# Optimization experiments

Hardware: AMD Instinct MI355X
Metric: run time of the kernel (lower is better)

The kernel has to match this reference:

```python
import jax, jax.numpy as jnp
import numpy as np

TOP_K = 20
BN_EPS = 1e-5

B, F, D, O = 2048, 16384, 512, 4096


def setup_inputs() -> dict:
    key = jax.random.key(0)
    ks = jax.random.split(key, 4)
    return {
        "sae_features": jax.random.uniform(ks[0], (B, F), jnp.float32),  # nonneg SAE activations
        "emb": jax.random.normal(ks[1], (F, D), jnp.float32) * (1.0 / np.sqrt(D)),
        "lin_w": jax.random.normal(ks[2], (O, F), jnp.float32) * (1.0 / np.sqrt(F)),
        "lin_b": jnp.zeros((O,), jnp.float32),
        "global_bias": jnp.zeros((O,), jnp.float32),
        "bn1_gamma": jnp.ones((D,), jnp.float32),
        "bn1_beta": jnp.zeros((D,), jnp.float32),
        "mlp_w1": jax.random.normal(ks[3], (D, D), jnp.float32) * np.sqrt(2.0 / D),
        "mlp_b1": jnp.zeros((D,), jnp.float32),
        "bn2_gamma": jnp.ones((D,), jnp.float32),
        "bn2_beta": jnp.zeros((D,), jnp.float32),
        "mlp_w2": jax.random.normal(jax.random.fold_in(key, 7), (O, D), jnp.float32) * np.sqrt(2.0 / D),
        "mlp_b2": jnp.zeros((O,), jnp.float32),
    }


def _batchnorm(x, gamma, beta):
    # training-mode BatchNorm1d: biased batch statistics, eps=1e-5
    mean = jnp.mean(x, axis=0)
    var = jnp.var(x, axis=0)
    return (x - mean) * jax.lax.rsqrt(var + BN_EPS) * gamma + beta


def reference(sae_features, emb, lin_w, lin_b, global_bias, bn1_gamma, bn1_beta,
              mlp_w1, mlp_b1, bn2_gamma, bn2_beta, mlp_w2, mlp_b2):
    b = sae_features.shape[0]
    # --- top-k sparsification (keep top 20 activations per row, zero the rest) ---
    top_vals, top_idx = jax.lax.top_k(sae_features, TOP_K)  # [B, K]
    x = jnp.zeros_like(sae_features).at[jnp.arange(b)[:, None], top_idx].set(top_vals)
    # --- bi-interaction pooling: 0.5*((x@E)^2 - (x^2)@(E^2)) ---
    # algebraically identical to the broadcast multiply-sum in the source
    sum_emb = x @ emb                      # [B, D]
    sum_sq = (x * x) @ (emb * emb)          # [B, D]
    bi = 0.5 * (sum_emb * sum_emb - sum_sq)
    # --- BN + interaction MLP (dropout = identity in eval) ---
    h = _batchnorm(bi, bn1_gamma, bn1_beta)
    h = h @ mlp_w1.T + mlp_b1
    h = jax.nn.relu(_batchnorm(h, bn2_gamma, bn2_beta))
    interaction_out = h @ mlp_w2.T + mlp_b2  # [B, O]
    # --- linear component on the ORIGINAL (non-sparsified) features ---
    linear_out = sae_features @ lin_w.T + lin_b  # [B, O]
    output = global_bias[None, :] + linear_out + interaction_out
    return output, linear_out, interaction_out
```

## Files before the change

kernel.cpp:

```cpp
#include <hip/hip_runtime.h>

#define B_ 2048
#define F_ 16384
#define D_ 512
#define O_ 4096

typedef __attribute__((ext_vector_type(8))) short bf16x8;
typedef __attribute__((ext_vector_type(4))) float f32x4;
typedef unsigned long long ull;

__device__ inline unsigned short f2bf(float f) {
    unsigned u = __float_as_uint(f);
    u += 0x7FFFu + ((u >> 16) & 1u);
    return (unsigned short)(u >> 16);
}

__device__ inline void glds16(const void* g, void* l) {
    __builtin_amdgcn_global_load_lds((const __attribute__((address_space(1))) void*)g,
                                     (__attribute__((address_space(3))) void*)l, 16, 0, 0);
}

__device__ inline void cvt_span(const float* __restrict__ s, unsigned short* __restrict__ d,
                                int n4, int tid0, int stride) {
    for (int i = tid0; i < n4; i += stride) {
        float4 v = ((const float4*)s)[i];
        ushort4 o;
        o.x = f2bf(v.x); o.y = f2bf(v.y); o.z = f2bf(v.z); o.w = f2bf(v.w);
        ((ushort4*)d)[i] = o;
    }
}

#define TOPK_BLKS (8 * B_)
#define CVT_BLKS  4096
__global__ __launch_bounds__(256) void fused_front_kernel(
        const float* __restrict__ sae, ull* __restrict__ cand,
        unsigned short* __restrict__ sae_bf,
        const float* __restrict__ lin_w, unsigned short* __restrict__ linw_bf,
        const float* __restrict__ w1, unsigned short* __restrict__ w1_bf,
        const float* __restrict__ w2, unsigned short* __restrict__ w2_bf) {
    __shared__ ull maxk[256];
    __shared__ ull cbuf[160];
    int tid = threadIdx.x;
    int bidx = blockIdx.x;
    if (bidx >= TOPK_BLKS) {
        int cb = bidx - TOPK_BLKS;
        int tid0 = cb * 256 + tid;
        int stride = CVT_BLKS * 256;
        cvt_span(lin_w, linw_bf, (int)((size_t)O_ * F_ / 4), tid0, stride);
        cvt_span(w1, w1_bf, D_ * D_ / 4, tid0, stride);
        cvt_span(w2, w2_bf, O_ * D_ / 4, tid0, stride);
        return;
    }
    int chunk = bidx & 7, row = bidx >> 3;
    size_t rbase = (size_t)row * F_ + chunk * 2048;
    const float4* src4 = (const float4*)(sae + rbase);
    ushort4* dst4 = (ushort4*)(sae_bf + rbase);

    float4 va = src4[tid], vb = src4[tid + 256];
    ushort4 oa, ob;
    oa.x = f2bf(va.x); oa.y = f2bf(va.y); oa.z = f2bf(va.z); oa.w = f2bf(va.w);
    ob.x = f2bf(vb.x); ob.y = f2bf(vb.y); ob.z = f2bf(vb.z); ob.w = f2bf(vb.w);
    dst4[tid] = oa; dst4[tid + 256] = ob;

    int c0 = chunk * 2048 + 4 * tid;
#define MKKEY(v, c) ((((ull)__float_as_uint(v)) << 32) | (unsigned)(~(c)))
    ull k0 = MKKEY(va.x, c0 + 0), k1 = MKKEY(va.y, c0 + 1);
    ull k2 = MKKEY(va.z, c0 + 2), k3 = MKKEY(va.w, c0 + 3);
    ull k4 = MKKEY(vb.x, c0 + 1024), k5 = MKKEY(vb.y, c0 + 1025);
    ull k6 = MKKEY(vb.z, c0 + 1026), k7 = MKKEY(vb.w, c0 + 1027);
#undef MKKEY
#define CE(a, b) { ull x_ = a, y_ = b; ull h_ = x_ > y_ ? x_ : y_; ull l_ = x_ > y_ ? y_ : x_; a = h_; b = l_; }
    CE(k0,k1) CE(k2,k3) CE(k4,k5) CE(k6,k7)
    CE(k0,k2) CE(k1,k3) CE(k4,k6) CE(k5,k7)
    CE(k1,k2) CE(k5,k6)
    CE(k0,k4) CE(k1,k5) CE(k2,k6) CE(k3,k7)
    CE(k2,k4) CE(k3,k5)
    CE(k1,k2) CE(k3,k4) CE(k5,k6)
#undef CE

    maxk[tid] = k0;
    __syncthreads();
    int r = 0;
    for (int k = 0; k < 256; ++k) r += (maxk[k] > k0);
    if (r < 20) {
        ull* o = cbuf + r * 8;
        o[0]=k0; o[1]=k1; o[2]=k2; o[3]=k3; o[4]=k4; o[5]=k5; o[6]=k6; o[7]=k7;
    }
    __syncthreads();
    ull myc = (tid < 160) ? cbuf[tid] : 0ull;
    int r2 = 0;
    for (int k = 0; k < 160; ++k) r2 += (cbuf[k] > myc);
    if (tid < 160 && r2 < 20)
        cand[((size_t)row * 8 + chunk) * 20 + r2] = myc;
}

__global__ __launch_bounds__(256) void bi_kernel(const ull* __restrict__ cand,
        const float* __restrict__ emb, float* __restrict__ bi) {
    __shared__ ull c[160];
    __shared__ int   si[20];
    __shared__ float sv[20];
    int tid = threadIdx.x, row = blockIdx.x;
    if (tid < 160) c[tid] = cand[(size_t)row * 160 + tid];
    __syncthreads();
    if (tid < 160) {
        ull m = c[tid];
        int r = 0;
        for (int k = 0; k < 160; ++k) r += (c[k] > m);
        if (r < 20) {
            sv[r] = __uint_as_float((unsigned)(m >> 32));
            si[r] = (int)(~(unsigned)m);
        }
    }
    __syncthreads();
    float s0 = 0.f, q0 = 0.f, s1 = 0.f, q1 = 0.f;
    int d0 = tid, d1 = tid + 256;
#pragma unroll
    for (int k = 0; k < 20; ++k) {
        float v = sv[k];
        const float* e = emb + (size_t)si[k] * D_;
        float e0 = e[d0], e1 = e[d1];
        s0 += v * e0; q0 += v * v * e0 * e0;
        s1 += v * e1; q1 += v * v * e1 * e1;
    }
    bi[(size_t)row * D_ + d0] = 0.5f * (s0 * s0 - q0);
    bi[(size_t)row * D_ + d1] = 0.5f * (s1 * s1 - q1);
}

__global__ __launch_bounds__(256) void colpart_kernel(const float* __restrict__ X,
        float* __restrict__ ps, float* __restrict__ pq, int N) {
    __shared__ float4 ls[128], lq[128];
    int tid = threadIdx.x;
    int c4 = tid & 127, half = tid >> 7;
    int r0 = blockIdx.x * 32 + half;
    float4 s = {0.f, 0.f, 0.f, 0.f}, q = {0.f, 0.f, 0.f, 0.f};
#pragma unroll
    for (int i = 0; i < 16; ++i) {
        float4 x = ((const float4*)(X + (size_t)(r0 + 2 * i) * N))[c4];
        s.x += x.x; s.y += x.y; s.z += x.z; s.w += x.w;
        q.x += x.x * x.x; q.y += x.y * x.y; q.z += x.z * x.z; q.w += x.w * x.w;
    }
    if (half) { ls[c4] = s; lq[c4] = q; }
    __syncthreads();
    if (!half) {
        float4 s2 = ls[c4], q2 = lq[c4];
        s.x += s2.x; s.y += s2.y; s.z += s2.z; s.w += s2.w;
        q.x += q2.x; q.y += q2.y; q.z += q2.z; q.w += q2.w;
        ((float4*)(ps + (size_t)blockIdx.x * N))[c4] = s;
        ((float4*)(pq + (size_t)blockIdx.x * N))[c4] = q;
    }
}

__global__ __launch_bounds__(256) void colfin_kernel(const float* __restrict__ ps,
        const float* __restrict__ pq, const float* __restrict__ gamma,
        const float* __restrict__ beta, float* __restrict__ scale,
        float* __restrict__ shift, int npart, int N, int M) {
    int col = blockIdx.x * 256 + threadIdx.x;
    if (col >= N) return;
    float s = 0.f, q = 0.f;
    for (int k = 0; k < npart; ++k) {
        s += ps[(size_t)k * N + col];
        q += pq[(size_t)k * N + col];
    }
    float mean = s / M;
    float var = q / M - mean * mean;
    float sc = gamma[col] * rsqrtf(var + 1e-5f);
    scale[col] = sc;
    shift[col] = beta[col] - mean * sc;
}

__global__ void bn_apply_kernel(const float* __restrict__ X, const float* __restrict__ scale,
        const float* __restrict__ shift, unsigned short* __restrict__ Y,
        int n4, int colmask4, int relu) {
    int stride = gridDim.x * blockDim.x;
    for (int i = blockIdx.x * blockDim.x + threadIdx.x; i < n4; i += stride) {
        float4 x = ((const float4*)X)[i];
        int c = (i & colmask4) * 4;
        float4 sc = *(const float4*)(scale + c);
        float4 sh = *(const float4*)(shift + c);
        float y0 = x.x * sc.x + sh.x;
        float y1 = x.y * sc.y + sh.y;
        float y2 = x.z * sc.z + sh.z;
        float y3 = x.w * sc.w + sh.w;
        if (relu) {
            y0 = fmaxf(y0, 0.f); y1 = fmaxf(y1, 0.f);
            y2 = fmaxf(y2, 0.f); y3 = fmaxf(y3, 0.f);
        }
        ushort4 o;
        o.x = f2bf(y0); o.y = f2bf(y1); o.z = f2bf(y2); o.w = f2bf(y3);
        ((ushort4*)Y)[i] = o;
    }
}

template <bool FUSE>
__global__ __launch_bounds__(512) void gemm8w_kernel(const unsigned short* __restrict__ A,
        const unsigned short* __restrict__ W, const float* __restrict__ bias,
        float* __restrict__ out, const float* __restrict__ lin,
        const float* __restrict__ gb, float* __restrict__ out0,
        int M, int N, int K) {
    __shared__ short As[3 * 4096];
    __shared__ short Bs[3 * 4096];
    int tid = threadIdx.x;
    int lane = tid & 63, w = tid >> 6;
    int wr = w >> 2, wc = w & 3;
    int l15 = lane & 15, lhi = lane >> 4;
    int xk = (l15 >> 1) & 3;
    int rchunk = (lhi ^ xk) << 3;

    int nwg = gridDim.x * gridDim.y;
    int bid = blockIdx.y * gridDim.x + blockIdx.x;
    int s = (bid & 7) * (nwg >> 3) + (bid >> 3);
    int gsz = gridDim.x << 3;
    int g = s / gsz, r = s % gsz;
    int by = (g << 3) + (r & 7);
    int bx = r >> 3;
    int bm = by * 128, bn = bx * 128;

    int rA = tid >> 2;
    int kp = tid & 3;
    int kps = kp ^ ((rA >> 1) & 3);
    const unsigned short* gA = A + (size_t)(bm + rA) * K + kps * 8;
    const unsigned short* gB = W + (size_t)(bn + rA) * K + kps * 8;

    f32x4 acc[4][2];
#pragma unroll
    for (int i = 0; i < 4; ++i)
#pragma unroll
        for (int j = 0; j < 2; ++j) { f32x4 z = {0.f, 0.f, 0.f, 0.f}; acc[i][j] = z; }

    auto STAGE = [&](int t, int buf) {
        int k0 = t << 5;
        glds16(gA + k0, (char*)(As + buf * 4096) + w * 1024);
        glds16(gB + k0, (char*)(Bs + buf * 4096) + w * 1024);
    };
    auto LOADF = [&](bf16x8* af, bf16x8* bv, int buf) {
        const short* Ab = As + buf * 4096;
        const short* Bb = Bs + buf * 4096;
#pragma unroll
        for (int mi = 0; mi < 4; ++mi)
            af[mi] = *(const bf16x8*)&Ab[(wr * 64 + mi * 16 + l15) * 32 + rchunk];
#pragma unroll
        for (int ni = 0; ni < 2; ++ni)
            bv[ni] = *(const bf16x8*)&Bb[(wc * 32 + ni * 16 + l15) * 32 + rchunk];
    };
    auto MFMA8 = [&](const bf16x8* af, const bf16x8* bv) {
#pragma unroll
        for (int mi = 0; mi < 4; ++mi)
#pragma unroll
            for (int ni = 0; ni < 2; ++ni)
                acc[mi][ni] = __builtin_amdgcn_mfma_f32_16x16x32_bf16(af[mi], bv[ni], acc[mi][ni], 0, 0, 0);
    };

    int NT = K >> 5;

    STAGE(0, 0);
    STAGE(1, 1);
    asm volatile("s_waitcnt vmcnt(2)" ::: "memory");
    __builtin_amdgcn_sched_barrier(0);
    __builtin_amdgcn_s_barrier();
    __builtin_amdgcn_sched_barrier(0);

    bf16x8 afA[4], bvA[2], afB[4], bvB[2];
    LOADF(afA, bvA, 0);

    for (int t = 0; t + 4 <= NT; t += 2) {
        STAGE(t + 2, (t + 2) % 3);
        asm volatile("s_waitcnt lgkmcnt(0)" ::: "memory");
        __builtin_amdgcn_sched_barrier(0);
        asm volatile("s_waitcnt vmcnt(2)" ::: "memory");
        __builtin_amdgcn_sched_barrier(0);
        __builtin_amdgcn_s_barrier();
        __builtin_amdgcn_sched_barrier(0);
        LOADF(afB, bvB, (t + 1) % 3);
        __builtin_amdgcn_s_setprio(1);
        MFMA8(afA, bvA);
        __builtin_amdgcn_s_setprio(0);
        __builtin_amdgcn_sched_group_barrier(0x100, 6, 0);
        __builtin_amdgcn_sched_group_barrier(0x008, 8, 0);
        STAGE(t + 3, (t + 3) % 3);
        asm volatile("s_waitcnt lgkmcnt(0)" ::: "memory");
        __builtin_amdgcn_sched_barrier(0);
        asm volatile("s_waitcnt vmcnt(2)" ::: "memory");
        __builtin_amdgcn_sched_barrier(0);
        __builtin_amdgcn_s_barrier();
        __builtin_amdgcn_sched_barrier(0);
        LOADF(afA, bvA, (t + 2) % 3);
        __builtin_amdgcn_s_setprio(1);
        MFMA8(afB, bvB);
        __builtin_amdgcn_s_setprio(0);
        __builtin_amdgcn_sched_group_barrier(0x100, 6, 0);
        __builtin_amdgcn_sched_group_barrier(0x008, 8, 0);
    }
    asm volatile("s_waitcnt lgkmcnt(0)" ::: "memory");
    __builtin_amdgcn_sched_barrier(0);
    asm volatile("s_waitcnt vmcnt(0)" ::: "memory");
    __builtin_amdgcn_sched_barrier(0);
    __builtin_amdgcn_s_barrier();
    __builtin_amdgcn_sched_barrier(0);
    LOADF(afB, bvB, (NT - 1) % 3);
    __builtin_amdgcn_s_setprio(1);
    MFMA8(afA, bvA);
    __builtin_amdgcn_s_setprio(0);
    asm volatile("s_waitcnt lgkmcnt(0)" ::: "memory");
    __builtin_amdgcn_sched_barrier(0);
    __builtin_amdgcn_s_setprio(1);
    MFMA8(afB, bvB);
    __builtin_amdgcn_s_setprio(0);

#pragma unroll
    for (int mi = 0; mi < 4; ++mi)
#pragma unroll
        for (int ni = 0; ni < 2; ++ni) {
            int col = bn + wc * 32 + ni * 16 + l15;
            float bb = bias[col];
            float gbv = FUSE ? gb[col] : 0.f;
            int row0 = bm + wr * 64 + mi * 16 + lhi * 4;
#pragma unroll
            for (int r2 = 0; r2 < 4; ++r2) {
                size_t idx = (size_t)(row0 + r2) * N + col;
                float v = acc[mi][ni][r2] + bb;
                out[idx] = v;
                if (FUSE) out0[idx] = gbv + lin[idx] + v;
            }
        }
}

template <bool FUSE>
__global__ __launch_bounds__(512) void gemm256_kernel(const unsigned short* __restrict__ A,
        const unsigned short* __restrict__ W, const float* __restrict__ bias,
        float* __restrict__ out, const float* __restrict__ lin,
        const float* __restrict__ gb, float* __restrict__ out0,
        int M, int N, int K) {
    __shared__ short As[3 * 16384];
    __shared__ short Bs[3 * 8192];
    int tid = threadIdx.x;
    int l = tid & 63, w = tid >> 6;
    int wm = w >> 1, wn = w & 1;
    int l15 = l & 15, lhi = l >> 4;
    int lr = l >> 3, lc = l & 7;
    int sc = lc ^ lr;

    int bid = blockIdx.y * gridDim.x + blockIdx.x;
    int s = (bid & 7) * ((gridDim.x * gridDim.y) >> 3) + (bid >> 3);
    int by = s & 7, bx = s >> 3;
    int bm = by * 256, bn = bx * 128;

    const unsigned short* gA0 = A + (size_t)(bm +   0 + w * 8 + lr) * K + sc * 8;
    const unsigned short* gA1 = A + (size_t)(bm +  64 + w * 8 + lr) * K + sc * 8;
    const unsigned short* gA2 = A + (size_t)(bm + 128 + w * 8 + lr) * K + sc * 8;
    const unsigned short* gA3 = A + (size_t)(bm + 192 + w * 8 + lr) * K + sc * 8;
    const unsigned short* gB0 = W + (size_t)(bn +   0 + w * 8 + lr) * K + sc * 8;
    const unsigned short* gB1 = W + (size_t)(bn +  64 + w * 8 + lr) * K + sc * 8;

    int xk7 = l15 & 7;
    int aR0 = (wm * 64 +  0 + l15) << 7;
    int aR1 = (wm * 64 + 16 + l15) << 7;
    int aR2 = (wm * 64 + 32 + l15) << 7;
    int aR3 = (wm * 64 + 48 + l15) << 7;
    int bR0 = (wn * 64 +  0 + l15) << 7;
    int bR1 = (wn * 64 + 16 + l15) << 7;
    int bR2 = (wn * 64 + 32 + l15) << 7;
    int bR3 = (wn * 64 + 48 + l15) << 7;
    int c0 = ((0 + lhi) ^ xk7) << 4;
    int c1 = ((4 + lhi) ^ xk7) << 4;

    f32x4 acc[4][4];
#pragma unroll
    for (int i = 0; i < 4; ++i)
#pragma unroll
        for (int j = 0; j < 4; ++j) { f32x4 z = {0.f, 0.f, 0.f, 0.f}; acc[i][j] = z; }

    const char* AsB = (const char*)As;
    const char* BsB = (const char*)Bs;
#define RDA(rr, cc, bo) (*(const bf16x8*)(AsB + (bo) + (rr) + (cc)))
#define RDB(rr, cc, bo) (*(const bf16x8*)(BsB + (bo) + (rr) + (cc)))
#define MM(x, y, ai, bi_) acc[ai][bi_] = __builtin_amdgcn_mfma_f32_16x16x32_bf16(x, y, acc[ai][bi_], 0, 0, 0);

    bf16x8 a0, a1, a2, a3, b0, b1, b2, b3;
    bf16x8 a4, a5, a6, a7, b4, b5, b6, b7;
#define SB    __builtin_amdgcn_sched_barrier(0);
#define BAR   { __builtin_amdgcn_s_barrier(); SB }

    int NT = K >> 6;

    {
        int dA = w * 1024;
        glds16(gA0, (char*)As + dA);           glds16(gA1, (char*)As + 8192 + dA);
        glds16(gA2, (char*)As + 16384 + dA);   glds16(gA3, (char*)As + 24576 + dA);
        glds16(gB0, (char*)Bs + dA);           glds16(gB1, (char*)Bs + 8192 + dA);
        glds16(gA0 + 64, (char*)As + 32768 + dA);         glds16(gA1 + 64, (char*)As + 32768 + 8192 + dA);
        glds16(gA2 + 64, (char*)As + 32768 + 16384 + dA); glds16(gA3 + 64, (char*)As + 32768 + 24576 + dA);
        glds16(gB0 + 64, (char*)Bs + 16384 + dA);         glds16(gB1 + 64, (char*)Bs + 16384 + 8192 + dA);
    }
    asm volatile("s_waitcnt vmcnt(6)" ::: "memory");
    SB
    BAR;

    int cur = 0;
    for (int t = 0; t < NT; ++t) {
        int s2 = cur + 2; if (s2 >= 3) s2 -= 3;
        int Abo = cur * 32768, Bbo = cur * 16384;
        int AboS = s2 * 32768, BboS = s2 * 16384;
        int kst = (t + 2) << 6;
        bool st = (t + 2) < NT;
        int dA = w * 1024;

        a0 = RDA(aR0, c0, Abo); a1 = RDA(aR1, c0, Abo);
        b0 = RDB(bR0, c0, Bbo); b1 = RDB(bR1, c0, Bbo);
        SB
        a2 = RDA(aR2, c0, Abo); a3 = RDA(aR3, c0, Abo);
        b2 = RDB(bR2, c0, Bbo); b3 = RDB(bR3, c0, Bbo);
        SB
        a4 = RDA(aR0, c1, Abo); a5 = RDA(aR1, c1, Abo);
        b4 = RDB(bR0, c1, Bbo); b5 = RDB(bR1, c1, Bbo);
        SB
        a6 = RDA(aR2, c1, Abo); a7 = RDA(aR3, c1, Abo);
        b6 = RDB(bR2, c1, Bbo); b7 = RDB(bR3, c1, Bbo);
        SB
        if (st) {
            glds16(gA0 + kst, (char*)As + AboS + dA);
            glds16(gA1 + kst, (char*)As + AboS + 8192 + dA);
            glds16(gA2 + kst, (char*)As + AboS + 16384 + dA);
            glds16(gA3 + kst, (char*)As + AboS + 24576 + dA);
            glds16(gB0 + kst, (char*)Bs + BboS + dA);
            glds16(gB1 + kst, (char*)Bs + BboS + 8192 + dA);
        }
        SB
        asm volatile("s_waitcnt lgkmcnt(12)" ::: "memory"); SB
        __builtin_amdgcn_s_setprio(1);
        MM(a0, b0, 0, 0) MM(a0, b1, 0, 1) MM(a1, b0, 1, 0) MM(a1, b1, 1, 1)
        __builtin_amdgcn_s_setprio(0); SB
        asm volatile("s_waitcnt lgkmcnt(8)" ::: "memory"); SB
        __builtin_amdgcn_s_setprio(1);
        MM(a2, b0, 2, 0) MM(a2, b1, 2, 1) MM(a3, b0, 3, 0) MM(a3, b1, 3, 1)
        MM(a0, b2, 0, 2) MM(a0, b3, 0, 3) MM(a1, b2, 1, 2) MM(a1, b3, 1, 3)
        MM(a2, b2, 2, 2) MM(a2, b3, 2, 3) MM(a3, b2, 3, 2) MM(a3, b3, 3, 3)
        __builtin_amdgcn_s_setprio(0); SB
        asm volatile("s_waitcnt lgkmcnt(4)" ::: "memory"); SB
        __builtin_amdgcn_s_setprio(1);
        MM(a4, b4, 0, 0) MM(a4, b5, 0, 1) MM(a5, b4, 1, 0) MM(a5, b5, 1, 1)
        __builtin_amdgcn_s_setprio(0); SB
        asm volatile("s_waitcnt lgkmcnt(0)" ::: "memory"); SB
        __builtin_amdgcn_s_setprio(1);
        MM(a6, b4, 2, 0) MM(a6, b5, 2, 1) MM(a7, b4, 3, 0) MM(a7, b5, 3, 1)
        MM(a4, b6, 0, 2) MM(a4, b7, 0, 3) MM(a5, b6, 1, 2) MM(a5, b7, 1, 3)
        MM(a6, b6, 2, 2) MM(a6, b7, 2, 3) MM(a7, b6, 3, 2) MM(a7, b7, 3, 3)
        __builtin_amdgcn_s_setprio(0);
        if (t + 1 < NT) {
            if (t + 2 < NT) { asm volatile("s_waitcnt vmcnt(6)" ::: "memory"); }
            else            { asm volatile("s_waitcnt vmcnt(0)" ::: "memory"); }
            SB
            BAR;
        }
        ++cur; if (cur >= 3) cur = 0;
    }
#undef RDA
#undef RDB
#undef MM
#undef SB
#undef BAR

#pragma unroll
    for (int mi = 0; mi < 4; ++mi)
#pragma unroll
        for (int ni = 0; ni < 4; ++ni) {
            int col = bn + wn * 64 + ni * 16 + l15;
            float bb = bias[col];
            float gbv = FUSE ? gb[col] : 0.f;
            int row0 = bm + wm * 64 + mi * 16 + lhi * 4;
#pragma unroll
            for (int r2 = 0; r2 < 4; ++r2) {
                size_t idx = (size_t)(row0 + r2) * N + col;
                float v = acc[mi][ni][r2] + bb;
                out[idx] = v;
                if (FUSE) out0[idx] = gbv + lin[idx] + v;
            }
        }
}

extern "C" void kernel_launch(void* const* d_in, const int* in_sizes, int n_in,
                              void* d_out, int out_size, void* d_ws, size_t ws_size,
                              hipStream_t stream) {
    const float* sae  = (const float*)d_in[0];
    const float* emb  = (const float*)d_in[1];
    const float* lin_w = (const float*)d_in[2];
    const float* lin_b = (const float*)d_in[3];
    const float* gbias = (const float*)d_in[4];
    const float* bn1g = (const float*)d_in[5];
    const float* bn1b = (const float*)d_in[6];
    const float* w1   = (const float*)d_in[7];
    const float* b1   = (const float*)d_in[8];
    const float* bn2g = (const float*)d_in[9];
    const float* bn2b = (const float*)d_in[10];
    const float* w2   = (const float*)d_in[11];
    const float* b2   = (const float*)d_in[12];
    float* out = (float*)d_out;
    const size_t BO = (size_t)B_ * O_;

    char* ws = (char*)d_ws;
    auto alloc = [&](size_t bytes) -> char* {
        char* p = ws;
        ws += (bytes + 255) & ~(size_t)255;
        return p;
    };
    unsigned short* sae_bf  = (unsigned short*)alloc((size_t)B_ * F_ * 2);
    unsigned short* linw_bf = (unsigned short*)alloc((size_t)O_ * F_ * 2);
    unsigned short* w1_bf   = (unsigned short*)alloc((size_t)D_ * D_ * 2);
    unsigned short* w2_bf   = (unsigned short*)alloc((size_t)O_ * D_ * 2);
    unsigned short* a1_bf   = (unsigned short*)alloc((size_t)B_ * D_ * 2);
    unsigned short* h2_bf   = (unsigned short*)alloc((size_t)B_ * D_ * 2);
    ull*   cand = (ull*)alloc((size_t)B_ * 160 * 8);
    float* bi = (float*)alloc((size_t)B_ * D_ * 4);
    float* h1 = (float*)alloc((size_t)B_ * D_ * 4);
    float* ps = (float*)alloc(64 * D_ * 4);
    float* pq = (float*)alloc(64 * D_ * 4);
    float* sc1 = (float*)alloc(D_ * 4);
    float* sh1 = (float*)alloc(D_ * 4);
    float* sc2 = (float*)alloc(D_ * 4);
    float* sh2 = (float*)alloc(D_ * 4);

    fused_front_kernel<<<TOPK_BLKS + CVT_BLKS, 256, 0, stream>>>(
        sae, cand, sae_bf, lin_w, linw_bf, w1, w1_bf, w2, w2_bf);

    bi_kernel<<<B_, 256, 0, stream>>>(cand, emb, bi);

    colpart_kernel<<<64, 256, 0, stream>>>(bi, ps, pq, D_);
    colfin_kernel<<<2, 256, 0, stream>>>(ps, pq, bn1g, bn1b, sc1, sh1, 64, D_, B_);
    bn_apply_kernel<<<1024, 256, 0, stream>>>(bi, sc1, sh1, a1_bf, B_ * D_ / 4, D_ / 4 - 1, 0);
    gemm8w_kernel<false><<<dim3(D_ / 128, B_ / 128), 512, 0, stream>>>(
        a1_bf, w1_bf, b1, h1, nullptr, nullptr, nullptr, B_, D_, D_);

    colpart_kernel<<<64, 256, 0, stream>>>(h1, ps, pq, D_);
    colfin_kernel<<<2, 256, 0, stream>>>(ps, pq, bn2g, bn2b, sc2, sh2, 64, D_, B_);
    bn_apply_kernel<<<1024, 256, 0, stream>>>(h1, sc2, sh2, h2_bf, B_ * D_ / 4, D_ / 4 - 1, 1);

    gemm256_kernel<false><<<dim3(O_ / 128, B_ / 256), 512, 0, stream>>>(
        sae_bf, linw_bf, lin_b, out + BO, nullptr, nullptr, nullptr, B_, O_, F_);

    gemm256_kernel<true><<<dim3(O_ / 128, B_ / 256), 512, 0, stream>>>(
        h2_bf, w2_bf, b2, out + 2 * BO, out + BO, gbias, out, B_, O_, D_);
}
```

Before: 547.7 us.

## Use 256x256-tile split-K GEMM for linear path, reduce partials in fused epilogue

The large sae@lin_w GEMM moves to a new kernel with 256x256 tiles and a split-K of 2 along blockIdx.z. Each half writes its own fp32 partial (bias added only in the first), and the FUSE epilogue of the interaction GEMM sums the two partials, writes linear_out back, and forms the final output. The larger tile raises arithmetic intensity, and split-K keeps the grid at 256 blocks to fill the CUs. The cost is an extra 32MB fp32 partial buffer that must be written and read back, plus higher register pressure from a 32-accumulator tile per thread.

```diff
diff --git a/kernel.cpp b/kernel.cpp
--- a/kernel.cpp
+++ b/kernel.cpp
@@ -327,7 +327,7 @@
 template <bool FUSE>
 __global__ __launch_bounds__(512) void gemm256_kernel(const unsigned short* __restrict__ A,
         const unsigned short* __restrict__ W, const float* __restrict__ bias,
-        float* __restrict__ out, const float* __restrict__ lin,
+        float* __restrict__ out, float* __restrict__ lin, const float* __restrict__ p1f,
         const float* __restrict__ gb, float* __restrict__ out0,
         int M, int N, int K) {
     __shared__ short As[3 * 16384];
@@ -472,7 +472,138 @@
                 size_t idx = (size_t)(row0 + r2) * N + col;
                 float v = acc[mi][ni][r2] + bb;
                 out[idx] = v;
-                if (FUSE) out0[idx] = gbv + lin[idx] + v;
+                if (FUSE) {
+                    float lf = lin[idx] + p1f[idx];
+                    lin[idx] = lf;
+                    out0[idx] = gbv + lf + v;
+                }
+            }
+        }
+}
+
+__global__ __launch_bounds__(512) void gemmSQ_kernel(const unsigned short* __restrict__ A,
+        const unsigned short* __restrict__ W, const float* __restrict__ bias,
+        float* __restrict__ out, float* __restrict__ p1,
+        int M, int N, int K_len, int ld) {
+    __shared__ short As[3 * 8192];
+    __shared__ short Bs[3 * 8192];
+    int tid = threadIdx.x;
+    int l = tid & 63, w = tid >> 6;
+    int wm = w >> 2, wn = w & 3;
+    int l15 = l & 15, lhi = l >> 4;
+    int kps = (l & 3) ^ ((l >> 3) & 3);
+    int z = blockIdx.z;
+    float* outz = z ? p1 : out;
+
+    int bid = blockIdx.y * gridDim.x + blockIdx.x;
+    int s = (bid & 7) * ((gridDim.x * gridDim.y) >> 3) + (bid >> 3);
+    int by = s & 7, bx = s >> 3;
+    int bm = by * 256, bn = bx * 256;
+
+    size_t koff = (size_t)z * K_len;
+    int srow = w * 16 + (l >> 2);
+    const unsigned short* gA0 = A + (size_t)(bm + srow) * ld + koff + kps * 8;
+    const unsigned short* gA1 = A + (size_t)(bm + srow + 128) * ld + koff + kps * 8;
+    const unsigned short* gB0 = W + (size_t)(bn + srow) * ld + koff + kps * 8;
+    const unsigned short* gB1 = W + (size_t)(bn + srow + 128) * ld + koff + kps * 8;
+
+    int ck = (lhi ^ ((l15 >> 1) & 3)) << 4;
+    int aR[8], bR[4];
+#pragma unroll
+    for (int mi = 0; mi < 8; ++mi) aR[mi] = (wm * 128 + mi * 16 + l15) * 64;
+#pragma unroll
+    for (int ni = 0; ni < 4; ++ni) bR[ni] = (wn * 64 + ni * 16 + l15) * 64;
+
+    f32x4 acc[8][4];
+#pragma unroll
+    for (int i = 0; i < 8; ++i)
+#pragma unroll
+        for (int j = 0; j < 4; ++j) { f32x4 zz = {0.f, 0.f, 0.f, 0.f}; acc[i][j] = zz; }
+
+    const char* AsB = (const char*)As;
+    const char* BsB = (const char*)Bs;
+#define SB    __builtin_amdgcn_sched_barrier(0);
+#define BAR   { __builtin_amdgcn_s_barrier(); SB }
+#define MM(x, y, ai, bi_) acc[ai][bi_] = __builtin_amdgcn_mfma_f32_16x16x32_bf16(x, y, acc[ai][bi_], 0, 0, 0);
+
+    auto STAGE = [&](int t, int buf) {
+        int k0 = t << 5;
+        glds16(gA0 + k0, (char*)As + buf * 16384 + w * 1024);
+        glds16(gA1 + k0, (char*)As + buf * 16384 + 8192 + w * 1024);
+        glds16(gB0 + k0, (char*)Bs + buf * 16384 + w * 1024);
+        glds16(gB1 + k0, (char*)Bs + buf * 16384 + 8192 + w * 1024);
+    };
+
+    bf16x8 a[8], b[4];
+    int NT = K_len >> 5;
+
+    STAGE(0, 0);
+    STAGE(1, 1);
+    asm volatile("s_waitcnt vmcnt(4)" ::: "memory");
+    SB
+    BAR;
+
+    int cur = 0;
+    for (int t = 0; t < NT; ++t) {
+        int s2 = cur + 2; if (s2 >= 3) s2 -= 3;
+        int Abo = cur * 16384, Bbo = cur * 16384;
+        int AboS = s2 * 16384, BboS = s2 * 16384;
+        int kst = (t + 2) << 5;
+        bool st = (t + 2) < NT;
+
+        a[0] = *(const bf16x8*)(AsB + Abo + aR[0] + ck);
+        a[1] = *(const bf16x8*)(AsB + Abo + aR[1] + ck);
+        a[2] = *(const bf16x8*)(AsB + Abo + aR[2] + ck);
+        a[3] = *(const bf16x8*)(AsB + Abo + aR[3] + ck);
+        b[0] = *(const bf16x8*)(BsB + Bbo + bR[0] + ck);
+        b[1] = *(const bf16x8*)(BsB + Bbo + bR[1] + ck);
+        SB
+        a[4] = *(const bf16x8*)(AsB + Abo + aR[4] + ck);
+        a[5] = *(const bf16x8*)(AsB + Abo + aR[5] + ck);
+        a[6] = *(const bf16x8*)(AsB + Abo + aR[6] + ck);
+        a[7] = *(const bf16x8*)(AsB + Abo + aR[7] + ck);
+        b[2] = *(const bf16x8*)(BsB + Bbo + bR[2] + ck);
+        b[3] = *(const bf16x8*)(BsB + Bbo + bR[3] + ck);
+        SB
+        if (st) STAGE(t + 2, s2);
+        SB
+        asm volatile("s_waitcnt lgkmcnt(6)" ::: "memory"); SB
+        __builtin_amdgcn_s_setprio(1);
+        MM(a[0], b[0], 0, 0) MM(a[0], b[1], 0, 1) MM(a[1], b[0], 1, 0) MM(a[1], b[1], 1, 1)
+        MM(a[2], b[0], 2, 0) MM(a[2], b[1], 2, 1) MM(a[3], b[0], 3, 0) MM(a[3], b[1], 3, 1)
+        __builtin_amdgcn_s_setprio(0); SB
+        asm volatile("s_waitcnt lgkmcnt(0)" ::: "memory"); SB
+        __builtin_amdgcn_s_setprio(1);
+        MM(a[4], b[0], 4, 0) MM(a[4], b[1], 4, 1) MM(a[5], b[0], 5, 0) MM(a[5], b[1], 5, 1)
+        MM(a[6], b[0], 6, 0) MM(a[6], b[1], 6, 1) MM(a[7], b[0], 7, 0) MM(a[7], b[1], 7, 1)
+        MM(a[0], b[2], 0, 2) MM(a[0], b[3], 0, 3) MM(a[1], b[2], 1, 2) MM(a[1], b[3], 1, 3)
+        MM(a[2], b[2], 2, 2) MM(a[2], b[3], 2, 3) MM(a[3], b[2], 3, 2) MM(a[3], b[3], 3, 3)
+        MM(a[4], b[2], 4, 2) MM(a[4], b[3], 4, 3) MM(a[5], b[2], 5, 2) MM(a[5], b[3], 5, 3)
+        MM(a[6], b[2], 6, 2) MM(a[6], b[3], 6, 3) MM(a[7], b[2], 7, 2) MM(a[7], b[3], 7, 3)
+        __builtin_amdgcn_s_setprio(0);
+        if (t + 1 < NT) {
+            if (t + 2 < NT) { asm volatile("s_waitcnt vmcnt(4)" ::: "memory"); }
+            else            { asm volatile("s_waitcnt vmcnt(0)" ::: "memory"); }
+            SB
+            BAR;
+        }
+        ++cur; if (cur >= 3) cur = 0;
+    }
+#undef MM
+#undef SB
+#undef BAR
+
+#pragma unroll
+    for (int mi = 0; mi < 8; ++mi)
+#pragma unroll
+        for (int ni = 0; ni < 4; ++ni) {
+            int col = bn + wn * 64 + ni * 16 + l15;
+            float bb = z ? 0.f : bias[col];
+            int row0 = bm + wm * 128 + mi * 16 + lhi * 4;
+#pragma unroll
+            for (int r2 = 0; r2 < 4; ++r2) {
+                size_t idx = (size_t)(row0 + r2) * N + col;
+                outz[idx] = acc[mi][ni][r2] + bb;
             }
         }
 }
@@ -508,6 +639,7 @@
     unsigned short* w2_bf   = (unsigned short*)alloc((size_t)O_ * D_ * 2);
     unsigned short* a1_bf   = (unsigned short*)alloc((size_t)B_ * D_ * 2);
     unsigned short* h2_bf   = (unsigned short*)alloc((size_t)B_ * D_ * 2);
+    float* p1 = (float*)alloc(BO * 4);
     ull*   cand = (ull*)alloc((size_t)B_ * 160 * 8);
     float* bi = (float*)alloc((size_t)B_ * D_ * 4);
     float* h1 = (float*)alloc((size_t)B_ * D_ * 4);
@@ -533,9 +665,9 @@
     colfin_kernel<<<2, 256, 0, stream>>>(ps, pq, bn2g, bn2b, sc2, sh2, 64, D_, B_);
     bn_apply_kernel<<<1024, 256, 0, stream>>>(h1, sc2, sh2, h2_bf, B_ * D_ / 4, D_ / 4 - 1, 1);
 
-    gemm256_kernel<false><<<dim3(O_ / 128, B_ / 256), 512, 0, stream>>>(
-        sae_bf, linw_bf, lin_b, out + BO, nullptr, nullptr, nullptr, B_, O_, F_);
+    gemmSQ_kernel<<<dim3(O_ / 256, B_ / 256, 2), 512, 0, stream>>>(
+        sae_bf, linw_bf, lin_b, out + BO, p1, B_, O_, F_ / 2, F_);
 
     gemm256_kernel<true><<<dim3(O_ / 128, B_ / 256), 512, 0, stream>>>(
-        h2_bf, w2_bf, b2, out + 2 * BO, out + BO, gbias, out, B_, O_, D_);
-}
+        h2_bf, w2_bf, b2, out + 2 * BO, out + BO, p1, gbias, out, B_, O_, D_);
+}
```

New measurement: 564.0 us. 3.0% more time.
